# Performance work log

Hardware: AMD Instinct MI355X
Metric: run time of the kernel (lower is better)

## Reference

```python
import jax, jax.numpy as jnp
import numpy as np

B, V, D = 256, 4096, 64

def setup_inputs() -> dict:
    key = jax.random.key(0)
    k1, k2 = jax.random.split(key)
    fusion_fs = jax.random.normal(k1, (B, V, D), dtype=jnp.float32)
    lan_fs = jax.random.normal(k2, (B, 1, D), dtype=jnp.float32)
    return {"fusion_fs": fusion_fs, "lan_fs": lan_fs}

def reference(fusion_fs, lan_fs):
    # sim_map: [b, a, q=1, v]
    sim = jnp.einsum('avd,bqd->baqv', fusion_fs, lan_fs)
    top2, _ = jax.lax.top_k(sim, 2)          # [B, B, 1, 2], sorted descending
    top2 = jnp.squeeze(top2, axis=2)          # [B, B, 2]  (q == 1)
    max_sim_0 = top2[..., 0]                  # [B, B]
    max_sim_1 = top2[..., 1]                  # [B, B]
    b = max_sim_0.shape[0]
    # off-diagonal selection of max_sim_1 -> [B, B-1], row-major order
    i = jnp.arange(b)[:, None]
    j = jnp.arange(b - 1)[None, :]
    max_sim_1_off = max_sim_1[i, j + (j >= i)]
    logits = jnp.concatenate([max_sim_0, max_sim_1_off], axis=1)  # [B, 2B-1]
    # target_pred = argmax(eye) = arange(B); CE with mean reduction
    logp = jax.nn.log_softmax(logits, axis=1)
    labels = jnp.arange(b)
    loss = -jnp.mean(logp[labels, labels])
    return loss
```

## Files before the change

kernel.cpp:

```cpp
#include <hip/hip_runtime.h>
#include <math.h>

#define BB 256
#define VV 4096
#define DD 64
#define NCHUNK 32
#define CHB 8192

typedef __attribute__((ext_vector_type(8))) _Float16 f16x8;
typedef __attribute__((ext_vector_type(2))) __fp16 fp16x2;
typedef __attribute__((ext_vector_type(4))) float f32x4;
typedef __attribute__((address_space(3))) void lds_void_t;
typedef const __attribute__((address_space(1))) void gvoid_t;

__global__ __launch_bounds__(256) void topk_sim_kernel(
    const float* __restrict__ F, const float* __restrict__ lan,
    float* __restrict__ max0P, float* __restrict__ max1P)
{
  extern __shared__ __align__(16) char smem[];

  const int t = threadIdx.x;
  const int a       = blockIdx.x >> 2;
  const int quarter = blockIdx.x & 3;
  const int wave = t >> 6;
  const int lane = t & 63;
  const int cl = lane & 15;
  const int o  = lane >> 4;
  const int cg = wave;

  const char* gFa = (const char*)(F + (size_t)a * VV * DD
                                  + (size_t)quarter * 1024 * DD);

  f16x8 bf[4][2];
#pragma unroll
  for (int ct = 0; ct < 4; ++ct)
#pragma unroll
    for (int s = 0; s < 2; ++s) {
      const float* p = lan + (cg * 64 + ct * 16 + cl) * DD + s * 32 + o * 8;
      float4 u0 = *(const float4*)p, u1 = *(const float4*)(p + 4);
      union { f16x8 v; fp16x2 h[4]; } U;
      U.h[0] = __builtin_amdgcn_cvt_pkrtz(u0.x, u0.y);
      U.h[1] = __builtin_amdgcn_cvt_pkrtz(u0.z, u0.w);
      U.h[2] = __builtin_amdgcn_cvt_pkrtz(u1.x, u1.y);
      U.h[3] = __builtin_amdgcn_cvt_pkrtz(u1.z, u1.w);
      bf[ct][s] = U.v;
    }

  int soff[2];
#pragma unroll
  for (int i = 0; i < 2; ++i) {
    int row = wave * 8 + i * 4 + o;
    soff[i] = row * 256 + (cl ^ (row & 7)) * 16;
  }

  auto stage = [&](int ch, char* buf) {
    const char* g = gFa + (size_t)ch * CHB;
    char* dst = buf + wave * 2048;
#pragma unroll
    for (int i = 0; i < 2; ++i) {
      __builtin_amdgcn_global_load_lds(
          (gvoid_t*)(g + soff[i]),
          (lds_void_t*)(dst + i * 1024), 16, 0, 0);
    }
  };

  stage(0, smem);
  stage(1, smem + CHB);

  float m0[4], m1[4];
#pragma unroll
  for (int ct = 0; ct < 4; ++ct) { m0[ct] = -INFINITY; m1[ct] = -INFINITY; }

  auto compute = [&](const char* buf) {
#pragma unroll
    for (int rt = 0; rt < 2; ++rt) {
      const int row = rt * 16 + cl;
      const int rx = row & 7;
      const char* rp = buf + row * 256;
      float4 u00 = *(const float4*)(rp + ((((o * 2 + 0) ^ rx)) << 4));
      float4 u01 = *(const float4*)(rp + ((((o * 2 + 1) ^ rx)) << 4));
      float4 u10 = *(const float4*)(rp + ((8 + ((o * 2 + 0) ^ rx)) << 4));
      float4 u11 = *(const float4*)(rp + ((8 + ((o * 2 + 1) ^ rx)) << 4));
      union { f16x8 v; fp16x2 h[4]; } A0, A1;
      A0.h[0] = __builtin_amdgcn_cvt_pkrtz(u00.x, u00.y);
      A0.h[1] = __builtin_amdgcn_cvt_pkrtz(u00.z, u00.w);
      A0.h[2] = __builtin_amdgcn_cvt_pkrtz(u01.x, u01.y);
      A0.h[3] = __builtin_amdgcn_cvt_pkrtz(u01.z, u01.w);
      A1.h[0] = __builtin_amdgcn_cvt_pkrtz(u10.x, u10.y);
      A1.h[1] = __builtin_amdgcn_cvt_pkrtz(u10.z, u10.w);
      A1.h[2] = __builtin_amdgcn_cvt_pkrtz(u11.x, u11.y);
      A1.h[3] = __builtin_amdgcn_cvt_pkrtz(u11.z, u11.w);
#pragma unroll
      for (int ct = 0; ct < 4; ++ct) {
        f32x4 acc = {0.f, 0.f, 0.f, 0.f};
        acc = __builtin_amdgcn_mfma_f32_16x16x32_f16(A0.v, bf[ct][0], acc, 0, 0, 0);
        acc = __builtin_amdgcn_mfma_f32_16x16x32_f16(A1.v, bf[ct][1], acc, 0, 0, 0);
        float h1 = fmaxf(acc[0], acc[1]), q1 = fminf(acc[0], acc[1]);
        float h2 = fmaxf(acc[2], acc[3]), q2 = fminf(acc[2], acc[3]);
        float M0 = fmaxf(h1, h2);
        float M1 = fmaxf(fminf(h1, h2), fmaxf(q1, q2));
        float old0 = m0[ct];
        m0[ct] = fmaxf(old0, M0);
        m1[ct] = fmaxf(m1[ct], fmaxf(fminf(old0, M0), M1));
      }
    }
  };

#pragma unroll 1
  for (int ch = 0; ch < NCHUNK; ++ch) {
    if (ch + 2 < NCHUNK) {
      stage(ch + 2, smem + (size_t)((ch + 2) & 3) * CHB);
      asm volatile("s_waitcnt vmcnt(4)" ::: "memory");
    } else if (ch + 1 < NCHUNK) {
      asm volatile("s_waitcnt vmcnt(2)" ::: "memory");
    } else {
      asm volatile("s_waitcnt vmcnt(0)" ::: "memory");
    }
    __builtin_amdgcn_s_barrier();
    __builtin_amdgcn_sched_barrier(0);
    compute(smem + (size_t)(ch & 3) * CHB);
  }

#pragma unroll
  for (int ct = 0; ct < 4; ++ct) {
#pragma unroll
    for (int off = 16; off <= 32; off <<= 1) {
      float p0 = __shfl_xor(m0[ct], off);
      float p1 = __shfl_xor(m1[ct], off);
      float n1 = fmaxf(fminf(m0[ct], p0), fmaxf(m1[ct], p1));
      m0[ct] = fmaxf(m0[ct], p0);
      m1[ct] = n1;
    }
    if (lane < 16) {
      const int col = cg * 64 + ct * 16 + lane;
      max0P[((size_t)a * 4 + quarter) * BB + col] = m0[ct];
      max1P[((size_t)a * 4 + quarter) * BB + col] = m1[ct];
    }
  }
}

__global__ __launch_bounds__(256) void lse_kernel(
    const float* __restrict__ max0P, const float* __restrict__ max1P,
    float* __restrict__ lossb)
{
  __shared__ float red[256];
  __shared__ float diag;
  const int b = blockIdx.x;
  const int t = threadIdx.x;
  float M0 = -INFINITY, M1 = -INFINITY;
#pragma unroll
  for (int q = 0; q < 4; ++q) {
    float p0 = max0P[((size_t)t * 4 + q) * BB + b];
    float p1 = max1P[((size_t)t * 4 + q) * BB + b];
    float n1 = fmaxf(fminf(M0, p0), fmaxf(M1, p1));
    M0 = fmaxf(M0, p0);
    M1 = n1;
  }
  float x0 = M0;
  float x1 = (t == b) ? -INFINITY : M1;
  if (t == b) diag = x0;
  red[t] = fmaxf(x0, x1);
  __syncthreads();
  for (int s = 128; s > 0; s >>= 1) {
    if (t < s) red[t] = fmaxf(red[t], red[t + s]);
    __syncthreads();
  }
  float M = red[0];
  __syncthreads();
  float e = expf(x0 - M) + ((t == b) ? 0.0f : expf(x1 - M));
  red[t] = e;
  __syncthreads();
  for (int s = 128; s > 0; s >>= 1) {
    if (t < s) red[t] = red[t] + red[t + s];
    __syncthreads();
  }
  if (t == 0) lossb[b] = logf(red[0]) + M - diag;
}

__global__ __launch_bounds__(256) void mean_kernel(
    const float* __restrict__ lossb, float* __restrict__ out)
{
  __shared__ float red[256];
  const int t = threadIdx.x;
  red[t] = lossb[t];
  __syncthreads();
  for (int s = 128; s > 0; s >>= 1) {
    if (t < s) red[t] += red[t + s];
    __syncthreads();
  }
  if (t == 0) out[0] = red[0] * (1.0f / 256.0f);
}

extern "C" void kernel_launch(void* const* d_in, const int* in_sizes, int n_in,
                              void* d_out, int out_size, void* d_ws, size_t ws_size,
                              hipStream_t stream) {
  const float* F   = (const float*)d_in[0];
  const float* lan = (const float*)d_in[1];
  float* ws = (float*)d_ws;
  float* max0P = ws;
  float* max1P = ws + 262144;
  float* lossb = ws + 524288;

  const int shmem = 4 * CHB;
  hipFuncSetAttribute((const void*)topk_sim_kernel,
                      hipFuncAttributeMaxDynamicSharedMemorySize, shmem);
  topk_sim_kernel<<<1024, 256, shmem, stream>>>(F, lan, max0P, max1P);
  lse_kernel<<<256, 256, 0, stream>>>(max0P, max1P, lossb);
  mean_kernel<<<1, 256, 0, stream>>>(lossb, (float*)d_out);
}
```

Measured before the change: 78.56 us.

## Give each wave a private LDS ring and remove block barriers

Switches to one 512-thread block per batch item, where each wave streams its own 16-row slice through a private 4-deep LDS ring and handles 128 columns. This removes the workgroup s_barrier per chunk and deepens prefetch to three chunks. In exchange, paired waves load the same rows twice, so global/L2 traffic doubles, and the large LDS footprint limits residency to one block per CU.

```diff
diff --git a/kernel.cpp b/kernel.cpp
--- a/kernel.cpp
+++ b/kernel.cpp
@@ -4,8 +4,10 @@
 #define BB 256
 #define VV 4096
 #define DD 64
-#define NCHUNK 32
-#define CHB 8192
+#define NCH 64
+#define CHB 16384
+#define SLICE 4096
+#define RING 4
 
 typedef __attribute__((ext_vector_type(8))) _Float16 f16x8;
 typedef __attribute__((ext_vector_type(2))) __fp16 fp16x2;
@@ -13,30 +15,29 @@
 typedef __attribute__((address_space(3))) void lds_void_t;
 typedef const __attribute__((address_space(1))) void gvoid_t;
 
-__global__ __launch_bounds__(256) void topk_sim_kernel(
+__global__ __launch_bounds__(512) void topk_sim_kernel(
     const float* __restrict__ F, const float* __restrict__ lan,
     float* __restrict__ max0P, float* __restrict__ max1P)
 {
   extern __shared__ __align__(16) char smem[];
-
   const int t = threadIdx.x;
-  const int a       = blockIdx.x >> 2;
-  const int quarter = blockIdx.x & 3;
+  const int a = blockIdx.x;
   const int wave = t >> 6;
   const int lane = t & 63;
   const int cl = lane & 15;
   const int o  = lane >> 4;
-  const int cg = wave;
-
-  const char* gFa = (const char*)(F + (size_t)a * VV * DD
-                                  + (size_t)quarter * 1024 * DD);
-
-  f16x8 bf[4][2];
-#pragma unroll
-  for (int ct = 0; ct < 4; ++ct)
+  const int rg = wave >> 1;
+  const int hf = wave & 1;
+
+  char* mybuf = smem + (size_t)wave * (RING * SLICE);
+  const char* gFa = (const char*)(F + (size_t)a * VV * DD);
+
+  f16x8 bf[8][2];
+#pragma unroll
+  for (int ct = 0; ct < 8; ++ct)
 #pragma unroll
     for (int s = 0; s < 2; ++s) {
-      const float* p = lan + (cg * 64 + ct * 16 + cl) * DD + s * 32 + o * 8;
+      const float* p = lan + (hf * 128 + ct * 16 + cl) * DD + s * 32 + o * 8;
       float4 u0 = *(const float4*)p, u1 = *(const float4*)(p + 4);
       union { f16x8 v; fp16x2 h[4]; } U;
       U.h[0] = __builtin_amdgcn_cvt_pkrtz(u0.x, u0.y);
@@ -46,83 +47,79 @@
       bf[ct][s] = U.v;
     }
 
-  int soff[2];
-#pragma unroll
-  for (int i = 0; i < 2; ++i) {
-    int row = wave * 8 + i * 4 + o;
-    soff[i] = row * 256 + (cl ^ (row & 7)) * 16;
+  int soff[4];
+#pragma unroll
+  for (int i = 0; i < 4; ++i) {
+    int rl = i * 4 + o;
+    soff[i] = (rg * 16 + rl) * 256 + (cl ^ (rl & 7)) * 16;
   }
 
   auto stage = [&](int ch, char* buf) {
     const char* g = gFa + (size_t)ch * CHB;
-    char* dst = buf + wave * 2048;
-#pragma unroll
-    for (int i = 0; i < 2; ++i) {
+#pragma unroll
+    for (int i = 0; i < 4; ++i) {
       __builtin_amdgcn_global_load_lds(
           (gvoid_t*)(g + soff[i]),
-          (lds_void_t*)(dst + i * 1024), 16, 0, 0);
+          (lds_void_t*)(buf + i * 1024), 16, 0, 0);
     }
   };
 
-  stage(0, smem);
-  stage(1, smem + CHB);
-
-  float m0[4], m1[4];
-#pragma unroll
-  for (int ct = 0; ct < 4; ++ct) { m0[ct] = -INFINITY; m1[ct] = -INFINITY; }
+  stage(0, mybuf);
+  stage(1, mybuf + SLICE);
+  stage(2, mybuf + 2 * SLICE);
+
+  float m0[8], m1[8];
+#pragma unroll
+  for (int ct = 0; ct < 8; ++ct) { m0[ct] = -INFINITY; m1[ct] = -INFINITY; }
 
   auto compute = [&](const char* buf) {
-#pragma unroll
-    for (int rt = 0; rt < 2; ++rt) {
-      const int row = rt * 16 + cl;
-      const int rx = row & 7;
-      const char* rp = buf + row * 256;
-      float4 u00 = *(const float4*)(rp + ((((o * 2 + 0) ^ rx)) << 4));
-      float4 u01 = *(const float4*)(rp + ((((o * 2 + 1) ^ rx)) << 4));
-      float4 u10 = *(const float4*)(rp + ((8 + ((o * 2 + 0) ^ rx)) << 4));
-      float4 u11 = *(const float4*)(rp + ((8 + ((o * 2 + 1) ^ rx)) << 4));
-      union { f16x8 v; fp16x2 h[4]; } A0, A1;
-      A0.h[0] = __builtin_amdgcn_cvt_pkrtz(u00.x, u00.y);
-      A0.h[1] = __builtin_amdgcn_cvt_pkrtz(u00.z, u00.w);
-      A0.h[2] = __builtin_amdgcn_cvt_pkrtz(u01.x, u01.y);
-      A0.h[3] = __builtin_amdgcn_cvt_pkrtz(u01.z, u01.w);
-      A1.h[0] = __builtin_amdgcn_cvt_pkrtz(u10.x, u10.y);
-      A1.h[1] = __builtin_amdgcn_cvt_pkrtz(u10.z, u10.w);
-      A1.h[2] = __builtin_amdgcn_cvt_pkrtz(u11.x, u11.y);
-      A1.h[3] = __builtin_amdgcn_cvt_pkrtz(u11.z, u11.w);
-#pragma unroll
-      for (int ct = 0; ct < 4; ++ct) {
-        f32x4 acc = {0.f, 0.f, 0.f, 0.f};
-        acc = __builtin_amdgcn_mfma_f32_16x16x32_f16(A0.v, bf[ct][0], acc, 0, 0, 0);
-        acc = __builtin_amdgcn_mfma_f32_16x16x32_f16(A1.v, bf[ct][1], acc, 0, 0, 0);
-        float h1 = fmaxf(acc[0], acc[1]), q1 = fminf(acc[0], acc[1]);
-        float h2 = fmaxf(acc[2], acc[3]), q2 = fminf(acc[2], acc[3]);
-        float M0 = fmaxf(h1, h2);
-        float M1 = fmaxf(fminf(h1, h2), fmaxf(q1, q2));
-        float old0 = m0[ct];
-        m0[ct] = fmaxf(old0, M0);
-        m1[ct] = fmaxf(m1[ct], fmaxf(fminf(old0, M0), M1));
-      }
+    const int rx = cl & 7;
+    const char* rp = buf + cl * 256;
+    float4 u00 = *(const float4*)(rp + ((((o * 2 + 0) ^ rx)) << 4));
+    float4 u01 = *(const float4*)(rp + ((((o * 2 + 1) ^ rx)) << 4));
+    float4 u10 = *(const float4*)(rp + ((8 + ((o * 2 + 0) ^ rx)) << 4));
+    float4 u11 = *(const float4*)(rp + ((8 + ((o * 2 + 1) ^ rx)) << 4));
+    union { f16x8 v; fp16x2 h[4]; } A0, A1;
+    A0.h[0] = __builtin_amdgcn_cvt_pkrtz(u00.x, u00.y);
+    A0.h[1] = __builtin_amdgcn_cvt_pkrtz(u00.z, u00.w);
+    A0.h[2] = __builtin_amdgcn_cvt_pkrtz(u01.x, u01.y);
+    A0.h[3] = __builtin_amdgcn_cvt_pkrtz(u01.z, u01.w);
+    A1.h[0] = __builtin_amdgcn_cvt_pkrtz(u10.x, u10.y);
+    A1.h[1] = __builtin_amdgcn_cvt_pkrtz(u10.z, u10.w);
+    A1.h[2] = __builtin_amdgcn_cvt_pkrtz(u11.x, u11.y);
+    A1.h[3] = __builtin_amdgcn_cvt_pkrtz(u11.z, u11.w);
+#pragma unroll
+    for (int ct = 0; ct < 8; ++ct) {
+      f32x4 acc = {0.f, 0.f, 0.f, 0.f};
+      acc = __builtin_amdgcn_mfma_f32_16x16x32_f16(A0.v, bf[ct][0], acc, 0, 0, 0);
+      acc = __builtin_amdgcn_mfma_f32_16x16x32_f16(A1.v, bf[ct][1], acc, 0, 0, 0);
+      float h1 = fmaxf(acc[0], acc[1]), q1 = fminf(acc[0], acc[1]);
+      float h2 = fmaxf(acc[2], acc[3]), q2 = fminf(acc[2], acc[3]);
+      float M0 = fmaxf(h1, h2);
+      float M1 = fmaxf(fminf(h1, h2), fmaxf(q1, q2));
+      float old0 = m0[ct];
+      m0[ct] = fmaxf(old0, M0);
+      m1[ct] = fmaxf(m1[ct], fmaxf(fminf(old0, M0), M1));
     }
   };
 
 #pragma unroll 1
-  for (int ch = 0; ch < NCHUNK; ++ch) {
-    if (ch + 2 < NCHUNK) {
-      stage(ch + 2, smem + (size_t)((ch + 2) & 3) * CHB);
-      asm volatile("s_waitcnt vmcnt(4)" ::: "memory");
-    } else if (ch + 1 < NCHUNK) {
-      asm volatile("s_waitcnt vmcnt(2)" ::: "memory");
+  for (int ch = 0; ch < NCH; ++ch) {
+    if (ch + 3 < NCH) {
+      stage(ch + 3, mybuf + (size_t)((ch + 3) & 3) * SLICE);
+      asm volatile("s_waitcnt vmcnt(12)" ::: "memory");
     } else {
-      asm volatile("s_waitcnt vmcnt(0)" ::: "memory");
-    }
-    __builtin_amdgcn_s_barrier();
+      const int rem = NCH - 1 - ch;
+      if (rem == 2)      asm volatile("s_waitcnt vmcnt(8)" ::: "memory");
+      else if (rem == 1) asm volatile("s_waitcnt vmcnt(4)" ::: "memory");
+      else               asm volatile("s_waitcnt vmcnt(0)" ::: "memory");
+    }
     __builtin_amdgcn_sched_barrier(0);
-    compute(smem + (size_t)(ch & 3) * CHB);
-  }
-
-#pragma unroll
-  for (int ct = 0; ct < 4; ++ct) {
+    compute(mybuf + (size_t)(ch & 3) * SLICE);
+  }
+
+#pragma unroll
+  for (int ct = 0; ct < 8; ++ct) {
 #pragma unroll
     for (int off = 16; off <= 32; off <<= 1) {
       float p0 = __shfl_xor(m0[ct], off);
@@ -132,9 +129,9 @@
       m1[ct] = n1;
     }
     if (lane < 16) {
-      const int col = cg * 64 + ct * 16 + lane;
-      max0P[((size_t)a * 4 + quarter) * BB + col] = m0[ct];
-      max1P[((size_t)a * 4 + quarter) * BB + col] = m1[ct];
+      const int col = hf * 128 + ct * 16 + lane;
+      max0P[((size_t)a * 4 + rg) * BB + col] = m0[ct];
+      max1P[((size_t)a * 4 + rg) * BB + col] = m1[ct];
     }
   }
 }
@@ -201,10 +198,10 @@
   float* max1P = ws + 262144;
   float* lossb = ws + 524288;
 
-  const int shmem = 4 * CHB;
+  const int shmem = 8 * RING * SLICE;
   hipFuncSetAttribute((const void*)topk_sim_kernel,
                       hipFuncAttributeMaxDynamicSharedMemorySize, shmem);
-  topk_sim_kernel<<<1024, 256, shmem, stream>>>(F, lan, max0P, max1P);
+  topk_sim_kernel<<<256, 512, shmem, stream>>>(F, lan, max0P, max1P);
   lse_kernel<<<256, 256, 0, stream>>>(max0P, max1P, lossb);
   mean_kernel<<<1, 256, 0, stream>>>(lossb, (float*)d_out);
 }
```

Result: slower. 94.55 us (+20.4%).
